# Kernel optimization log

Measured on AMD Instinct MI355X. Metric: run time of the kernel, lower is better.

## Reference

```python
import jax, jax.numpy as jnp
import numpy as np

TEMPERATURE = 0.07
BASE_TEMPERATURE = 0.07
LAMBDA_HARD = 1.0
HMAX = 1.0
EPS = 1e-8
SIGMA = 0.5  # Gaussian RBF kernel bandwidth on label differences


def setup_inputs() -> dict:
    key = jax.random.key(0)
    kf, kl = jax.random.split(key)
    features = jax.random.normal(kf, (2048, 2, 128), dtype=jnp.float32)
    labels = jax.random.uniform(kl, (2048, 1), dtype=jnp.float32)
    return {"features": features, "labels": labels}


def reference(features, labels):
    bsz, n_views, dim = features.shape
    # L2-normalize each view's embedding (F.normalize, eps=1e-12)
    z = features / jnp.maximum(
        jnp.linalg.norm(features, axis=-1, keepdims=True), 1e-12
    )
    # torch.cat(torch.unbind(z, dim=1), dim=0) -> view-major stacking: [N, dim]
    z = jnp.concatenate([z[:, v, :] for v in range(n_views)], axis=0)
    y = jnp.tile(labels.reshape(-1, 1), (n_views, 1))  # [N, 1]
    N = y.shape[0]

    dy_raw = y - y.T                                   # [N, N] label diffs
    # kernel similarity weights w = K(y_i - y_k), clamped to [0, 1]
    w = jnp.clip(jnp.exp(-(dy_raw ** 2) / (2.0 * SIGMA ** 2)), 0.0, 1.0)

    d_y = jnp.abs(dy_raw)
    d_y = d_y / (d_y.max() + EPS)

    # cosine distance of unit vectors: 1 - z @ z.T
    sim_cos = z @ z.T                                  # [N, N]
    d_z = 1.0 - sim_cos
    d_z = d_z / (d_z.max() + EPS)

    u = jnp.clip(d_z - d_y, -HMAX, HMAX)
    m = 1.0 + LAMBDA_HARD * jax.nn.relu(u)
    n = 1.0 + LAMBDA_HARD * jax.nn.relu(-u)
    w_hat = w * m + (1.0 - w) * n                      # hardness-aware weights

    sim = sim_cos / TEMPERATURE                        # logits [N, N]
    logits_mask = 1.0 - jnp.eye(N, dtype=sim.dtype)
    exp_sim = jnp.exp(sim) * logits_mask
    pos = exp_sim * w_hat
    neg = exp_sim * (1.0 - w_hat)
    denom = (pos + neg).sum(axis=1, keepdims=True) + EPS

    log_prob = sim * w_hat - jnp.log(denom)
    pos_mask = w_hat * logits_mask
    mean_log_prob_pos = (pos_mask * log_prob).sum(axis=1) / (
        pos_mask.sum(axis=1) + EPS
    )
    loss = -(TEMPERATURE / BASE_TEMPERATURE) * mean_log_prob_pos
    return loss.mean()
```

## Files before the change

kernel.cpp:

```cpp
#include <hip/hip_runtime.h>
#include <hip/hip_bf16.h>

#define NROWS 4096
#define BSZ   2048
#define DIM   128

typedef __bf16 bf16x8 __attribute__((ext_vector_type(8)));
typedef float  f32x4  __attribute__((ext_vector_type(4)));

__global__ __launch_bounds__(256) void k_prep(const float* __restrict__ feats,
                                              const float* __restrict__ labels,
                                              __hip_bfloat16* __restrict__ zbf,
                                              float* __restrict__ y,
                                              float* __restrict__ scal) {
    int t = threadIdx.x;
    int p = blockIdx.x;
    int r = t >> 4;
    int c = t & 15;
    int i = p * 16 + r;
    int srow = (i < BSZ) ? i : (i - BSZ);
    int view = (i < BSZ) ? 0 : 1;
    const float* src = feats + ((size_t)srow * 2 + view) * DIM + c * 8;
    float4 v0 = *reinterpret_cast<const float4*>(src);
    float4 v1 = *reinterpret_cast<const float4*>(src + 4);
    float ss = v0.x*v0.x + v0.y*v0.y + v0.z*v0.z + v0.w*v0.w
             + v1.x*v1.x + v1.y*v1.y + v1.z*v1.z + v1.w*v1.w;
    #pragma unroll
    for (int off = 8; off >= 1; off >>= 1) ss += __shfl_xor(ss, off);
    float inv = 1.0f / fmaxf(sqrtf(ss), 1e-12f);
    bf16x8 hz;
    hz[0] = (__bf16)(v0.x * inv); hz[1] = (__bf16)(v0.y * inv);
    hz[2] = (__bf16)(v0.z * inv); hz[3] = (__bf16)(v0.w * inv);
    hz[4] = (__bf16)(v1.x * inv); hz[5] = (__bf16)(v1.y * inv);
    hz[6] = (__bf16)(v1.z * inv); hz[7] = (__bf16)(v1.w * inv);
    bf16x8* zv = (bf16x8*)zbf;
    zv[(size_t)p * 256 + (c >> 2) * 64 + (c & 3) * 16 + r] = hz;
    if (c == 0) y[i] = labels[srow];

    if (p == 0) {
        float mn = 1e30f, mx = -1e30f;
        for (int k = t; k < BSZ; k += 256) {
            float v = labels[k];
            mn = fminf(mn, v); mx = fmaxf(mx, v);
        }
        #pragma unroll
        for (int off = 32; off >= 1; off >>= 1) {
            mn = fminf(mn, __shfl_xor(mn, off));
            mx = fmaxf(mx, __shfl_xor(mx, off));
        }
        __shared__ float smn[4], smx[4];
        if ((t & 63) == 0) { smn[t >> 6] = mn; smx[t >> 6] = mx; }
        __syncthreads();
        if (t == 0) {
            mn = fminf(fminf(smn[0], smn[1]), fminf(smn[2], smn[3]));
            mx = fmaxf(fmaxf(smx[0], smx[1]), fmaxf(smx[2], smx[3]));
            scal[1] = mx - mn;
        }
    }
}

__global__ __launch_bounds__(256) void k_smin(const __hip_bfloat16* __restrict__ zbf,
                                              float* __restrict__ bmin) {
    int wv    = threadIdx.x >> 6;
    int lane  = threadIdx.x & 63;
    int strip = blockIdx.x * 4 + wv;
    const bf16x8* zv = (const bf16x8*)zbf;

    bf16x8 afr[4];
    #pragma unroll
    for (int kt = 0; kt < 4; ++kt)
        afr[kt] = zv[(size_t)strip * 256 + kt * 64 + lane];

    float mymin = 1e30f;
    #pragma unroll
    for (int t = 0; t < 16; ++t) {
        int p = blockIdx.y * 16 + t;
        bf16x8 bfr[4];
        #pragma unroll
        for (int kt = 0; kt < 4; ++kt)
            bfr[kt] = zv[(size_t)p * 256 + kt * 64 + lane];
        f32x4 acc = {0.f, 0.f, 0.f, 0.f};
        #pragma unroll
        for (int kt = 0; kt < 4; ++kt)
            acc = __builtin_amdgcn_mfma_f32_16x16x32_bf16(afr[kt], bfr[kt], acc, 0, 0, 0);
        #pragma unroll
        for (int j = 0; j < 4; ++j) mymin = fminf(mymin, acc[j]);
    }
    #pragma unroll
    for (int off = 32; off >= 1; off >>= 1)
        mymin = fminf(mymin, __shfl_xor(mymin, off));
    __shared__ float wmin[4];
    if (lane == 0) wmin[wv] = mymin;
    __syncthreads();
    if (threadIdx.x == 0)
        bmin[blockIdx.y * 64 + blockIdx.x] =
            fminf(fminf(wmin[0], wmin[1]), fminf(wmin[2], wmin[3]));
}

__global__ __launch_bounds__(256) void k_redmin(const float* __restrict__ bmin,
                                                float* __restrict__ scal) {
    int t = threadIdx.x;
    float mn = 1e30f;
    #pragma unroll
    for (int c = 0; c < 4; ++c) mn = fminf(mn, bmin[c * 256 + t]);
    #pragma unroll
    for (int off = 32; off >= 1; off >>= 1) mn = fminf(mn, __shfl_xor(mn, off));
    __shared__ float wmin[4];
    if ((t & 63) == 0) wmin[t >> 6] = mn;
    __syncthreads();
    if (t == 0)
        scal[0] = fminf(fminf(wmin[0], wmin[1]), fminf(wmin[2], wmin[3]));
}

__global__ __launch_bounds__(256) void k_main(const __hip_bfloat16* __restrict__ zbf,
                                              const float* __restrict__ y,
                                              const float* __restrict__ scal,
                                              float* __restrict__ partE,
                                              float* __restrict__ partS1,
                                              float* __restrict__ partS2) {
    int wv    = threadIdx.x >> 6;
    int lane  = threadIdx.x & 63;
    int strip = blockIdx.x * 4 + wv;
    int lrow  = lane & 15;
    int lk    = lane >> 4;

    float smin  = scal[0];
    float invdz = 1.0f / ((1.0f - smin) + 1e-8f);
    float invdy = 1.0f / (scal[1] + 1e-8f);
    const float invT = 1.0f / 0.07f;

    const bf16x8* zv = (const bf16x8*)zbf;
    bf16x8 afr[4];
    #pragma unroll
    for (int kt = 0; kt < 4; ++kt)
        afr[kt] = zv[(size_t)strip * 256 + kt * 64 + lane];

    int myrow0 = strip * 16 + lk * 4;
    float yr[4];
    #pragma unroll
    for (int j = 0; j < 4; ++j) yr[j] = y[myrow0 + j];

    float accE[4] = {0.f, 0.f, 0.f, 0.f};
    float acc1[4] = {0.f, 0.f, 0.f, 0.f};
    float acc2[4] = {0.f, 0.f, 0.f, 0.f};

    int c0 = blockIdx.y * 256;
    #pragma unroll
    for (int t = 0; t < 16; ++t) {
        int p = blockIdx.y * 16 + t;
        bf16x8 bfr[4];
        #pragma unroll
        for (int kt = 0; kt < 4; ++kt)
            bfr[kt] = zv[(size_t)p * 256 + kt * 64 + lane];
        float yc = y[c0 + t * 16 + lrow];
        f32x4 acc = {0.f, 0.f, 0.f, 0.f};
        #pragma unroll
        for (int kt = 0; kt < 4; ++kt)
            acc = __builtin_amdgcn_mfma_f32_16x16x32_bf16(afr[kt], bfr[kt], acc, 0, 0, 0);
        int mycol = c0 + t * 16 + lrow;
        #pragma unroll
        for (int j = 0; j < 4; ++j) {
            float s  = acc[j];
            bool  on = (myrow0 + j != mycol);
            float dy = yr[j] - yc;
            float w  = __expf(-2.0f * dy * dy);
            float dyn = fabsf(dy) * invdy;
            float dzn = (1.0f - s) * invdz;
            float u   = fminf(fmaxf(dzn - dyn, -1.0f), 1.0f);
            float wh  = (u > 0.0f) ? (1.0f + w * u) : (1.0f - (1.0f - w) * u);
            float sT  = s * invT;
            float e   = on ? __expf(sT) : 0.0f;
            float whm = on ? wh : 0.0f;
            accE[j] += e;
            acc1[j] += whm;
            acc2[j] += whm * wh * sT;
        }
    }
    #pragma unroll
    for (int j = 0; j < 4; ++j) {
        #pragma unroll
        for (int off = 1; off < 16; off <<= 1) {
            accE[j] += __shfl_xor(accE[j], off);
            acc1[j] += __shfl_xor(acc1[j], off);
            acc2[j] += __shfl_xor(acc2[j], off);
        }
    }
    if (lrow == 0) {
        size_t base = (size_t)blockIdx.y * NROWS + myrow0;
        f32x4 vE = {accE[0], accE[1], accE[2], accE[3]};
        f32x4 v1 = {acc1[0], acc1[1], acc1[2], acc1[3]};
        f32x4 v2 = {acc2[0], acc2[1], acc2[2], acc2[3]};
        *(f32x4*)&partE[base]  = vE;
        *(f32x4*)&partS1[base] = v1;
        *(f32x4*)&partS2[base] = v2;
    }
}

__global__ __launch_bounds__(256) void k_rowred(const float* __restrict__ partE,
                                                const float* __restrict__ partS1,
                                                const float* __restrict__ partS2,
                                                float* __restrict__ out) {
    int r = blockIdx.x * 256 + threadIdx.x;
    float E = 0.f, S1 = 0.f, S2 = 0.f;
    #pragma unroll
    for (int c = 0; c < 16; ++c) {
        size_t o = (size_t)c * NROWS + r;
        E  += partE[o];
        S1 += partS1[o];
        S2 += partS2[o];
    }
    float mlpp = (S2 - logf(E + 1e-8f) * S1) / (S1 + 1e-8f);
    float sum  = -mlpp;
    #pragma unroll
    for (int off = 32; off >= 1; off >>= 1) sum += __shfl_xor(sum, off);
    __shared__ float red[4];
    if ((threadIdx.x & 63) == 0) red[threadIdx.x >> 6] = sum;
    __syncthreads();
    if (threadIdx.x == 0)
        atomicAdd(out, (red[0] + red[1] + red[2] + red[3]) * (1.0f / NROWS));
}

extern "C" void kernel_launch(void* const* d_in, const int* in_sizes, int n_in,
                              void* d_out, int out_size, void* d_ws, size_t ws_size,
                              hipStream_t stream) {
    const float* feats  = (const float*)d_in[0];
    const float* labels = (const float*)d_in[1];
    float* out = (float*)d_out;

    char* ws = (char*)d_ws;
    __hip_bfloat16* zbf = (__hip_bfloat16*)ws;
    float* y      = (float*)(ws + (1 << 20));
    float* scal   = y + NROWS;
    float* bmin   = scal + 16;
    float* partE  = bmin + 1024;
    float* partS1 = partE  + 16 * NROWS;
    float* partS2 = partS1 + 16 * NROWS;

    hipMemsetAsync(out, 0, sizeof(float), stream);

    k_prep  <<<NROWS / 16, 256, 0, stream>>>(feats, labels, zbf, y, scal);
    dim3 g(64, 16);
    k_smin  <<<g, 256, 0, stream>>>(zbf, bmin);
    k_redmin<<<1, 256, 0, stream>>>(bmin, scal);
    k_main  <<<g, 256, 0, stream>>>(zbf, y, scal, partE, partS1, partS2);
    k_rowred<<<16, 256, 0, stream>>>(partE, partS1, partS2, out);
}
```

Baseline: 95.57 us.

## Fuse pipeline into one cooperative persistent kernel with grid syncs

New measurement: 342.3 us. +258.1%, slower.

```diff
diff --git a/kernel.cpp b/kernel.cpp
--- a/kernel.cpp
+++ b/kernel.cpp
@@ -1,22 +1,26 @@
 #include <hip/hip_runtime.h>
 #include <hip/hip_bf16.h>
+#include <hip/hip_cooperative_groups.h>
+
+namespace cg = cooperative_groups;
 
 #define NROWS 4096
 #define BSZ   2048
 #define DIM   128
+#define CB    512
+#define NTASK 4096
+#define COOPW (CB * 4)
 
 typedef __bf16 bf16x8 __attribute__((ext_vector_type(8)));
 typedef float  f32x4  __attribute__((ext_vector_type(4)));
 
-__global__ __launch_bounds__(256) void k_prep(const float* __restrict__ feats,
-                                              const float* __restrict__ labels,
-                                              __hip_bfloat16* __restrict__ zbf,
-                                              float* __restrict__ y,
-                                              float* __restrict__ scal) {
-    int t = threadIdx.x;
-    int p = blockIdx.x;
-    int r = t >> 4;
-    int c = t & 15;
+__device__ __forceinline__ void do_prep(int p, int tid,
+                                        const float* __restrict__ feats,
+                                        const float* __restrict__ labels,
+                                        __hip_bfloat16* __restrict__ zbf,
+                                        float* __restrict__ y) {
+    int r = tid >> 4;
+    int c = tid & 15;
     int i = p * 16 + r;
     int srow = (i < BSZ) ? i : (i - BSZ);
     int view = (i < BSZ) ? 0 : 1;
@@ -33,48 +37,45 @@
     hz[2] = (__bf16)(v0.z * inv); hz[3] = (__bf16)(v0.w * inv);
     hz[4] = (__bf16)(v1.x * inv); hz[5] = (__bf16)(v1.y * inv);
     hz[6] = (__bf16)(v1.z * inv); hz[7] = (__bf16)(v1.w * inv);
-    bf16x8* zv = (bf16x8*)zbf;
-    zv[(size_t)p * 256 + (c >> 2) * 64 + (c & 3) * 16 + r] = hz;
+    ((bf16x8*)zbf)[(size_t)p * 256 + (c >> 2) * 64 + (c & 3) * 16 + r] = hz;
     if (c == 0) y[i] = labels[srow];
-
-    if (p == 0) {
-        float mn = 1e30f, mx = -1e30f;
-        for (int k = t; k < BSZ; k += 256) {
-            float v = labels[k];
-            mn = fminf(mn, v); mx = fmaxf(mx, v);
-        }
-        #pragma unroll
-        for (int off = 32; off >= 1; off >>= 1) {
-            mn = fminf(mn, __shfl_xor(mn, off));
-            mx = fmaxf(mx, __shfl_xor(mx, off));
-        }
-        __shared__ float smn[4], smx[4];
-        if ((t & 63) == 0) { smn[t >> 6] = mn; smx[t >> 6] = mx; }
-        __syncthreads();
-        if (t == 0) {
-            mn = fminf(fminf(smn[0], smn[1]), fminf(smn[2], smn[3]));
-            mx = fmaxf(fmaxf(smx[0], smx[1]), fmaxf(smx[2], smx[3]));
-            scal[1] = mx - mn;
-        }
-    }
-}
-
-__global__ __launch_bounds__(256) void k_smin(const __hip_bfloat16* __restrict__ zbf,
-                                              float* __restrict__ bmin) {
-    int wv    = threadIdx.x >> 6;
-    int lane  = threadIdx.x & 63;
-    int strip = blockIdx.x * 4 + wv;
-    const bf16x8* zv = (const bf16x8*)zbf;
-
+}
+
+__device__ __forceinline__ void do_label_range(int tid,
+                                               const float* __restrict__ labels,
+                                               float* __restrict__ scal,
+                                               float* __restrict__ out,
+                                               float* smn, float* smx) {
+    float mn = 1e30f, mx = -1e30f;
+    for (int k = tid; k < BSZ; k += 256) {
+        float v = labels[k];
+        mn = fminf(mn, v); mx = fmaxf(mx, v);
+    }
+    #pragma unroll
+    for (int off = 32; off >= 1; off >>= 1) {
+        mn = fminf(mn, __shfl_xor(mn, off));
+        mx = fmaxf(mx, __shfl_xor(mx, off));
+    }
+    if ((tid & 63) == 0) { smn[tid >> 6] = mn; smx[tid >> 6] = mx; }
+    __syncthreads();
+    if (tid == 0) {
+        mn = fminf(fminf(smn[0], smn[1]), fminf(smn[2], smn[3]));
+        mx = fmaxf(fmaxf(smx[0], smx[1]), fmaxf(smx[2], smx[3]));
+        scal[1] = mx - mn;
+        out[0]  = 0.0f;
+    }
+}
+
+__device__ __forceinline__ float gram_task_min(int strip, int by, int lane,
+                                               const bf16x8* __restrict__ zv) {
     bf16x8 afr[4];
     #pragma unroll
     for (int kt = 0; kt < 4; ++kt)
         afr[kt] = zv[(size_t)strip * 256 + kt * 64 + lane];
-
     float mymin = 1e30f;
     #pragma unroll
-    for (int t = 0; t < 16; ++t) {
-        int p = blockIdx.y * 16 + t;
+    for (int u = 0; u < 16; ++u) {
+        int p = by * 16 + u;
         bf16x8 bfr[4];
         #pragma unroll
         for (int kt = 0; kt < 4; ++kt)
@@ -86,78 +87,44 @@
         #pragma unroll
         for (int j = 0; j < 4; ++j) mymin = fminf(mymin, acc[j]);
     }
-    #pragma unroll
-    for (int off = 32; off >= 1; off >>= 1)
-        mymin = fminf(mymin, __shfl_xor(mymin, off));
-    __shared__ float wmin[4];
-    if (lane == 0) wmin[wv] = mymin;
-    __syncthreads();
-    if (threadIdx.x == 0)
-        bmin[blockIdx.y * 64 + blockIdx.x] =
-            fminf(fminf(wmin[0], wmin[1]), fminf(wmin[2], wmin[3]));
-}
-
-__global__ __launch_bounds__(256) void k_redmin(const float* __restrict__ bmin,
-                                                float* __restrict__ scal) {
-    int t = threadIdx.x;
-    float mn = 1e30f;
-    #pragma unroll
-    for (int c = 0; c < 4; ++c) mn = fminf(mn, bmin[c * 256 + t]);
-    #pragma unroll
-    for (int off = 32; off >= 1; off >>= 1) mn = fminf(mn, __shfl_xor(mn, off));
-    __shared__ float wmin[4];
-    if ((t & 63) == 0) wmin[t >> 6] = mn;
-    __syncthreads();
-    if (t == 0)
-        scal[0] = fminf(fminf(wmin[0], wmin[1]), fminf(wmin[2], wmin[3]));
-}
-
-__global__ __launch_bounds__(256) void k_main(const __hip_bfloat16* __restrict__ zbf,
-                                              const float* __restrict__ y,
-                                              const float* __restrict__ scal,
-                                              float* __restrict__ partE,
-                                              float* __restrict__ partS1,
-                                              float* __restrict__ partS2) {
-    int wv    = threadIdx.x >> 6;
-    int lane  = threadIdx.x & 63;
-    int strip = blockIdx.x * 4 + wv;
-    int lrow  = lane & 15;
-    int lk    = lane >> 4;
-
-    float smin  = scal[0];
-    float invdz = 1.0f / ((1.0f - smin) + 1e-8f);
-    float invdy = 1.0f / (scal[1] + 1e-8f);
+    return mymin;
+}
+
+__device__ __forceinline__ void gram_task_main(int strip, int by, int lane,
+                                               const bf16x8* __restrict__ zv,
+                                               const float* __restrict__ y,
+                                               float invdz, float invdy,
+                                               float* __restrict__ partE,
+                                               float* __restrict__ partS1,
+                                               float* __restrict__ partS2) {
+    int lrow = lane & 15, lk = lane >> 4;
     const float invT = 1.0f / 0.07f;
-
-    const bf16x8* zv = (const bf16x8*)zbf;
     bf16x8 afr[4];
     #pragma unroll
     for (int kt = 0; kt < 4; ++kt)
         afr[kt] = zv[(size_t)strip * 256 + kt * 64 + lane];
-
     int myrow0 = strip * 16 + lk * 4;
     float yr[4];
     #pragma unroll
     for (int j = 0; j < 4; ++j) yr[j] = y[myrow0 + j];
 
-    float accE[4] = {0.f, 0.f, 0.f, 0.f};
-    float acc1[4] = {0.f, 0.f, 0.f, 0.f};
-    float acc2[4] = {0.f, 0.f, 0.f, 0.f};
-
-    int c0 = blockIdx.y * 256;
-    #pragma unroll
-    for (int t = 0; t < 16; ++t) {
-        int p = blockIdx.y * 16 + t;
+    float accE[4] = {0.f,0.f,0.f,0.f};
+    float acc1[4] = {0.f,0.f,0.f,0.f};
+    float acc2[4] = {0.f,0.f,0.f,0.f};
+    int c0 = by * 256;
+    #pragma unroll
+    for (int u = 0; u < 16; ++u) {
+        int p = by * 16 + u;
         bf16x8 bfr[4];
         #pragma unroll
         for (int kt = 0; kt < 4; ++kt)
             bfr[kt] = zv[(size_t)p * 256 + kt * 64 + lane];
-        float yc = y[c0 + t * 16 + lrow];
+        float yc = y[c0 + u * 16 + lrow];
         f32x4 acc = {0.f, 0.f, 0.f, 0.f};
         #pragma unroll
         for (int kt = 0; kt < 4; ++kt)
             acc = __builtin_amdgcn_mfma_f32_16x16x32_bf16(afr[kt], bfr[kt], acc, 0, 0, 0);
-        int mycol = c0 + t * 16 + lrow;
+        int mycol = c0 + u * 16 + lrow;
         #pragma unroll
         for (int j = 0; j < 4; ++j) {
             float s  = acc[j];
@@ -166,8 +133,8 @@
             float w  = __expf(-2.0f * dy * dy);
             float dyn = fabsf(dy) * invdy;
             float dzn = (1.0f - s) * invdz;
-            float u   = fminf(fmaxf(dzn - dyn, -1.0f), 1.0f);
-            float wh  = (u > 0.0f) ? (1.0f + w * u) : (1.0f - (1.0f - w) * u);
+            float uu  = fminf(fmaxf(dzn - dyn, -1.0f), 1.0f);
+            float wh  = (uu > 0.0f) ? (1.0f + w * uu) : (1.0f - (1.0f - w) * uu);
             float sT  = s * invT;
             float e   = on ? __expf(sT) : 0.0f;
             float whm = on ? wh : 0.0f;
@@ -186,7 +153,7 @@
         }
     }
     if (lrow == 0) {
-        size_t base = (size_t)blockIdx.y * NROWS + myrow0;
+        size_t base = (size_t)by * NROWS + myrow0;
         f32x4 vE = {accE[0], accE[1], accE[2], accE[3]};
         f32x4 v1 = {acc1[0], acc1[1], acc1[2], acc1[3]};
         f32x4 v2 = {acc2[0], acc2[1], acc2[2], acc2[3]};
@@ -196,11 +163,12 @@
     }
 }
 
-__global__ __launch_bounds__(256) void k_rowred(const float* __restrict__ partE,
-                                                const float* __restrict__ partS1,
-                                                const float* __restrict__ partS2,
-                                                float* __restrict__ out) {
-    int r = blockIdx.x * 256 + threadIdx.x;
+__device__ __forceinline__ void do_rowred(int blk, int tid,
+                                          const float* __restrict__ partE,
+                                          const float* __restrict__ partS1,
+                                          const float* __restrict__ partS2,
+                                          float* __restrict__ out, float* wred) {
+    int r = blk * 256 + tid;
     float E = 0.f, S1 = 0.f, S2 = 0.f;
     #pragma unroll
     for (int c = 0; c < 16; ++c) {
@@ -213,11 +181,135 @@
     float sum  = -mlpp;
     #pragma unroll
     for (int off = 32; off >= 1; off >>= 1) sum += __shfl_xor(sum, off);
-    __shared__ float red[4];
-    if ((threadIdx.x & 63) == 0) red[threadIdx.x >> 6] = sum;
+    if ((tid & 63) == 0) wred[tid >> 6] = sum;
+    __syncthreads();
+    if (tid == 0)
+        atomicAdd(out, (wred[0] + wred[1] + wred[2] + wred[3]) * (1.0f / NROWS));
+}
+
+__global__ __launch_bounds__(256, 4) void k_coop(const float* __restrict__ feats,
+                                                 const float* __restrict__ labels,
+                                                 __hip_bfloat16* __restrict__ zbf,
+                                                 float* __restrict__ y,
+                                                 float* __restrict__ scal,
+                                                 float* __restrict__ bmin,
+                                                 float* __restrict__ partE,
+                                                 float* __restrict__ partS1,
+                                                 float* __restrict__ partS2,
+                                                 float* __restrict__ out) {
+    cg::grid_group grid = cg::this_grid();
+    const int tid  = threadIdx.x;
+    const int bid  = blockIdx.x;
+    const int wv   = tid >> 6;
+    const int lane = tid & 63;
+    const bf16x8* zv = (const bf16x8*)zbf;
+    __shared__ float wred[4];
+    __shared__ float smx[4];
+    __shared__ float s_smin;
+
+    if (bid < 256) do_prep(bid, tid, feats, labels, zbf, y);
+    if (bid == 0)  do_label_range(tid, labels, scal, out, wred, smx);
+
+    grid.sync();
+
+    float mymin = 1e30f;
+    for (int t = bid * 4 + wv; t < NTASK; t += COOPW) {
+        int strip = t & 255, by = t >> 8;
+        if (by * 256 + 255 >= strip * 16)
+            mymin = fminf(mymin, gram_task_min(strip, by, lane, zv));
+    }
+    #pragma unroll
+    for (int off = 32; off >= 1; off >>= 1)
+        mymin = fminf(mymin, __shfl_xor(mymin, off));
+    if (lane == 0) wred[wv] = mymin;
+    __syncthreads();
+    if (tid == 0)
+        bmin[bid] = fminf(fminf(wred[0], wred[1]), fminf(wred[2], wred[3]));
+
+    grid.sync();
+
+    float m = fminf(bmin[tid], bmin[256 + tid]);
+    #pragma unroll
+    for (int off = 32; off >= 1; off >>= 1) m = fminf(m, __shfl_xor(m, off));
+    if (lane == 0) wred[wv] = m;
+    __syncthreads();
+    if (tid == 0)
+        s_smin = fminf(fminf(wred[0], wred[1]), fminf(wred[2], wred[3]));
+    __syncthreads();
+    float invdz = 1.0f / ((1.0f - s_smin) + 1e-8f);
+    float invdy = 1.0f / (scal[1] + 1e-8f);
+    for (int t = bid * 4 + wv; t < NTASK; t += COOPW) {
+        int strip = t & 255, by = t >> 8;
+        gram_task_main(strip, by, lane, zv, y, invdz, invdy, partE, partS1, partS2);
+    }
+
+    grid.sync();
+
+    if (bid < 16) do_rowred(bid, tid, partE, partS1, partS2, out, wred);
+}
+
+__global__ __launch_bounds__(256) void k_prep(const float* __restrict__ feats,
+                                              const float* __restrict__ labels,
+                                              __hip_bfloat16* __restrict__ zbf,
+                                              float* __restrict__ y,
+                                              float* __restrict__ scal,
+                                              float* __restrict__ out) {
+    __shared__ float smn[4], smx[4];
+    do_prep(blockIdx.x, threadIdx.x, feats, labels, zbf, y);
+    if (blockIdx.x == 0) do_label_range(threadIdx.x, labels, scal, out, smn, smx);
+}
+
+__global__ __launch_bounds__(256) void k_smin(const __hip_bfloat16* __restrict__ zbf,
+                                              float* __restrict__ bmin) {
+    int wv = threadIdx.x >> 6, lane = threadIdx.x & 63;
+    int strip = blockIdx.x * 4 + wv;
+    float mymin = (blockIdx.y * 256 + 255 >= strip * 16)
+                ? gram_task_min(strip, blockIdx.y, lane, (const bf16x8*)zbf)
+                : 1e30f;
+    #pragma unroll
+    for (int off = 32; off >= 1; off >>= 1)
+        mymin = fminf(mymin, __shfl_xor(mymin, off));
+    __shared__ float wmin[4];
+    if (lane == 0) wmin[wv] = mymin;
     __syncthreads();
     if (threadIdx.x == 0)
-        atomicAdd(out, (red[0] + red[1] + red[2] + red[3]) * (1.0f / NROWS));
+        bmin[blockIdx.y * 64 + blockIdx.x] =
+            fminf(fminf(wmin[0], wmin[1]), fminf(wmin[2], wmin[3]));
+}
+
+__global__ __launch_bounds__(256) void k_main(const __hip_bfloat16* __restrict__ zbf,
+                                              const float* __restrict__ y,
+                                              const float* __restrict__ scal,
+                                              const float* __restrict__ bmin,
+                                              float* __restrict__ partE,
+                                              float* __restrict__ partS1,
+                                              float* __restrict__ partS2) {
+    int tid = threadIdx.x, wv = tid >> 6, lane = tid & 63;
+    __shared__ float wred[4];
+    __shared__ float s_smin;
+    float m = 1e30f;
+    #pragma unroll
+    for (int c = 0; c < 4; ++c) m = fminf(m, bmin[c * 256 + tid]);
+    #pragma unroll
+    for (int off = 32; off >= 1; off >>= 1) m = fminf(m, __shfl_xor(m, off));
+    if (lane == 0) wred[wv] = m;
+    __syncthreads();
+    if (tid == 0)
+        s_smin = fminf(fminf(wred[0], wred[1]), fminf(wred[2], wred[3]));
+    __syncthreads();
+    float invdz = 1.0f / ((1.0f - s_smin) + 1e-8f);
+    float invdy = 1.0f / (scal[1] + 1e-8f);
+    int strip = blockIdx.x * 4 + wv;
+    gram_task_main(strip, blockIdx.y, lane, (const bf16x8*)zbf, y,
+                   invdz, invdy, partE, partS1, partS2);
+}
+
+__global__ __launch_bounds__(256) void k_rowred(const float* __restrict__ partE,
+                                                const float* __restrict__ partS1,
+                                                const float* __restrict__ partS2,
+                                                float* __restrict__ out) {
+    __shared__ float wred[4];
+    do_rowred(blockIdx.x, threadIdx.x, partE, partS1, partS2, out, wred);
 }
 
 extern "C" void kernel_launch(void* const* d_in, const int* in_sizes, int n_in,
@@ -236,12 +328,17 @@
     float* partS1 = partE  + 16 * NROWS;
     float* partS2 = partS1 + 16 * NROWS;
 
-    hipMemsetAsync(out, 0, sizeof(float), stream);
-
-    k_prep  <<<NROWS / 16, 256, 0, stream>>>(feats, labels, zbf, y, scal);
-    dim3 g(64, 16);
-    k_smin  <<<g, 256, 0, stream>>>(zbf, bmin);
-    k_redmin<<<1, 256, 0, stream>>>(bmin, scal);
-    k_main  <<<g, 256, 0, stream>>>(zbf, y, scal, partE, partS1, partS2);
-    k_rowred<<<16, 256, 0, stream>>>(partE, partS1, partS2, out);
-}
+    void* args[] = {(void*)&feats, (void*)&labels, (void*)&zbf, (void*)&y,
+                    (void*)&scal, (void*)&bmin, (void*)&partE, (void*)&partS1,
+                    (void*)&partS2, (void*)&out};
+    hipError_t err = hipLaunchCooperativeKernel((const void*)k_coop, dim3(CB),
+                                                dim3(256), args, 0, stream);
+    if (err != hipSuccess) {
+        (void)hipGetLastError();
+        k_prep  <<<NROWS / 16, 256, 0, stream>>>(feats, labels, zbf, y, scal, out);
+        dim3 g(64, 16);
+        k_smin  <<<g, 256, 0, stream>>>(zbf, bmin);
+        k_main  <<<g, 256, 0, stream>>>(zbf, y, scal, bmin, partE, partS1, partS2);
+        k_rowred<<<16, 256, 0, stream>>>(partE, partS1, partS2, out);
+    }
+}
```
